# Kernel optimization log

Hardware: AMD Instinct MI355X
Metric: run time of the kernel (lower is better)

Reference implementation:

```python
import jax, jax.numpy as jnp
import numpy as np

B, S, D, H, L, V, DF = 2, 1024, 1024, 16, 4, 32000, 4096


def setup_inputs() -> dict:
    key = jax.random.key(0)
    ks = iter(jax.random.split(key, 64))
    rn = lambda shape, s=0.02: jax.random.normal(next(ks), shape, jnp.float32) * s
    inp = {
        'dec_input': rn((B, S, D), 1.0),
        'enc_input': rn((B, S, D), 1.0),
        # additive masks: causal for self-attn, none for cross-attn
        'masked_attention_mask': jnp.where(jnp.tril(jnp.ones((S, S), bool)), 0.0, -1e9)[None, None].astype(jnp.float32),
        'cross_attention_mask': jnp.zeros((1, 1, S, S), jnp.float32),
        'num_heads': H,
    }
    for p in ['sWq', 'sWk', 'sWv', 'sWo', 'cWq', 'cWk', 'cWv', 'cWo']:
        inp[p] = rn((L, D, D))
    for p in ['sbq', 'sbk', 'sbv', 'sbo', 'cbq', 'cbk', 'cbv', 'cbo']:
        inp[p] = jnp.zeros((L, D), jnp.float32)
    for p in ['ln1_g', 'ln2_g', 'ln3_g']:
        inp[p] = jnp.ones((L, D), jnp.float32)
    for p in ['ln1_b', 'ln2_b', 'ln3_b']:
        inp[p] = jnp.zeros((L, D), jnp.float32)
    inp['fW1'] = rn((L, D, DF)); inp['fb1'] = jnp.zeros((L, DF), jnp.float32)
    inp['fW2'] = rn((L, DF, D)); inp['fb2'] = jnp.zeros((L, D), jnp.float32)
    inp['Wout'] = rn((D, V)); inp['bout'] = jnp.zeros((V,), jnp.float32)
    return inp


def positional_encoding(seq_len, d_model, n=10000.0):
    # vectorized equivalent of the original triple-nested loop:
    # even d -> sin(i / n^(d/D)); odd d -> cos(i / n^((d-1)/D)); d==0 denom 1 == n^0
    i = jnp.arange(seq_len, dtype=jnp.float32)[:, None]
    d = jnp.arange(d_model)
    denom = jnp.power(n, (2 * (d // 2)).astype(jnp.float32) / d_model)
    ang = i / denom
    return jnp.where(d % 2 == 0, jnp.sin(ang), jnp.cos(ang))  # [S, D]


def layer_norm(x, g, b, eps=1e-5):
    m = jnp.mean(x, -1, keepdims=True)
    v = jnp.mean(jnp.square(x - m), -1, keepdims=True)
    return (x - m) * jax.lax.rsqrt(v + eps) * g + b


def mha(q_in, k_in, v_in, mask, Wq, bq, Wk, bk, Wv, bv, Wo, bo, h):
    b, sq, d = q_in.shape
    dh = d // h
    q = (q_in @ Wq + bq).reshape(b, sq, h, dh)
    k = (k_in @ Wk + bk).reshape(b, -1, h, dh)
    v = (v_in @ Wv + bv).reshape(b, -1, h, dh)
    scores = jnp.einsum('bqhd,bkhd->bhqk', q, k) / jnp.sqrt(jnp.float32(dh)) + mask
    attn = jax.nn.softmax(scores, axis=-1)
    out = jnp.einsum('bhqk,bkhd->bqhd', attn, v).reshape(b, sq, d)
    return out @ Wo + bo


def reference(dec_input, enc_input, masked_attention_mask, cross_attention_mask,
              sWq, sbq, sWk, sbk, sWv, sbv, sWo, sbo,
              cWq, cbq, cWk, cbk, cWv, cbv, cWo, cbo,
              ln1_g, ln1_b, ln2_g, ln2_b, ln3_g, ln3_b,
              fW1, fb1, fW2, fb2, Wout, bout, num_heads):
    b, s, d = dec_input.shape
    x0 = dec_input + positional_encoding(s, d)
    n_layers = sWq.shape[0]
    y = x0
    for l in range(n_layers):
        # NOTE: original DecoderSequential bug: every block consumes the ORIGINAL input;
        # only the last block's output survives.
        a1 = layer_norm(x0 + mha(x0, x0, x0, masked_attention_mask,
                                 sWq[l], sbq[l], sWk[l], sbk[l], sWv[l], sbv[l], sWo[l], sbo[l], num_heads),
                        ln1_g[l], ln1_b[l])
        a2 = layer_norm(a1 + mha(a1, enc_input, enc_input, cross_attention_mask,
                                 cWq[l], cbq[l], cWk[l], cbk[l], cWv[l], cbv[l], cWo[l], cbo[l], num_heads),
                        ln2_g[l], ln2_b[l])
        ff = jax.nn.relu(a2 @ fW1[l] + fb1[l]) @ fW2[l] + fb2[l]
        y = layer_norm(a2 + ff, ln3_g[l], ln3_b[l])
    return y @ Wout + bout  # [B, S, V]
```

## Files before the change

### kernel.cpp

```cpp
#include <hip/hip_runtime.h>
#include <cstdint>
#include <cstddef>

#define DEV __device__ __forceinline__

typedef __attribute__((ext_vector_type(8))) short short8;
typedef __attribute__((ext_vector_type(4))) float f32x4;
typedef __attribute__((ext_vector_type(16))) float f32x16;
typedef __attribute__((ext_vector_type(4))) unsigned short ushort4v;

DEV unsigned short f2bf(float f){
  union { float f; unsigned int i; } v; v.f = f;
  unsigned int r = v.i + 0x7fffu + ((v.i >> 16) & 1u);
  return (unsigned short)(r >> 16);
}

DEV void gld_lds16(const unsigned short* g, unsigned short* lds){
  __builtin_amdgcn_global_load_lds((const __attribute__((address_space(1))) void*)g,
                                   (__attribute__((address_space(3))) void*)lds, 16, 0, 0);
}

template<int BN, int EPI>
__global__ __launch_bounds__(256, 2)
void gemm32(const unsigned short* __restrict__ A,
            const unsigned short* __restrict__ Bt,
            const float* __restrict__ bias,
            void* __restrict__ C, int M, int N, int K)
{
  constexpr int NFR  = BN / 64;
  constexpr int ROWS = 128 + BN;
  constexpr int BUFH = ROWS * 32;
  constexpr int GLD  = ROWS / 64;
  __shared__ __align__(16) unsigned short lds[3 * BUFH];

  const int tid = threadIdx.x, wid = tid >> 6, l = tid & 63;
  const int wr = wid >> 1, wcn = wid & 1;

  const int nbm = M / 128, nbn = N / BN;
  const int nwg = nbm * nbn;
  const int q8 = nwg >> 3, r8 = nwg & 7;
  const int xcd = blockIdx.x & 7, within = blockIdx.x >> 3;
  const int wg = (xcd < r8 ? xcd * (q8 + 1) : r8 * (q8 + 1) + (xcd - r8) * q8) + within;
  const int mb = (wg % nbm) * 128, nb = (wg / nbm) * BN;

  const int nk = K / 32;

  const int r31 = l & 31, hi = l >> 5;
  const int so0 = (( hi)      ^ (r31 & 3)) * 8;
  const int so1 = ((2 + hi)   ^ (r31 & 3)) * 8;
  const int abase = (wr * 64 + r31) * 32;
  const int bbase = 4096 + (wcn * (BN / 2) + r31) * 32;

  f32x16 acc[2][NFR];
  #pragma unroll
  for (int m = 0; m < 2; m++)
    #pragma unroll
    for (int n = 0; n < NFR; n++)
      #pragma unroll
      for (int e = 0; e < 16; e++) acc[m][n][e] = 0.f;

#define STAGE_A(c, tt, bb) \
  gld_lds16(A + (size_t)(mb + (c)*64 + (tid>>2)) * K + (size_t)(tt)*32 + (((tid&3)^((tid>>2)&3))*8), \
            lds + (bb)*BUFH + (c)*2048 + tid*8)
#define STAGE_B(c, tt, bb) \
  gld_lds16(Bt + (size_t)(nb + (c)*64 + (tid>>2)) * K + (size_t)(tt)*32 + (((tid&3)^((tid>>2)&3))*8), \
            lds + (bb)*BUFH + 4096 + (c)*2048 + tid*8)
#define WAIT_GLD() do { if constexpr (GLD == 6) asm volatile("s_waitcnt vmcnt(6)" ::: "memory"); \
                        else                    asm volatile("s_waitcnt vmcnt(4)" ::: "memory"); } while(0)

  STAGE_A(0, 0, 0); STAGE_A(1, 0, 0);
  #pragma unroll
  for (int c = 0; c < NFR; c++) STAGE_B(c, 0, 0);
  if (nk > 1){
    STAGE_A(0, 1, 1); STAGE_A(1, 1, 1);
    #pragma unroll
    for (int c = 0; c < NFR; c++) STAGE_B(c, 1, 1);
    WAIT_GLD();
  } else {
    asm volatile("s_waitcnt vmcnt(0)" ::: "memory");
  }
  asm volatile("" ::: "memory");
  __builtin_amdgcn_s_barrier();
  asm volatile("" ::: "memory");

  int bb = 0;
  for (int u = 0; u < nk; u++){
    const unsigned short* buf = lds + bb * BUFH;
    const int sb = (bb >= 1) ? bb - 1 : 2;
    const bool st = (u + 2 < nk);
    short8 af[2], bf[NFR];

    af[0] = *(const short8*)(buf + abase + so0);
    af[1] = *(const short8*)(buf + abase + 1024 + so0);
    #pragma unroll
    for (int n = 0; n < NFR; n++) bf[n] = *(const short8*)(buf + bbase + n * 1024 + so0);
    if (st){
      STAGE_A(0, u + 2, sb); STAGE_A(1, u + 2, sb);
      if constexpr (NFR == 4) STAGE_B(0, u + 2, sb);
    }
    __builtin_amdgcn_s_setprio(1);
    #pragma unroll
    for (int m = 0; m < 2; m++)
      #pragma unroll
      for (int n = 0; n < NFR; n++)
        acc[m][n] = __builtin_amdgcn_mfma_f32_32x32x16_bf16(af[m], bf[n], acc[m][n], 0, 0, 0);
    __builtin_amdgcn_s_setprio(0);

    af[0] = *(const short8*)(buf + abase + so1);
    af[1] = *(const short8*)(buf + abase + 1024 + so1);
    #pragma unroll
    for (int n = 0; n < NFR; n++) bf[n] = *(const short8*)(buf + bbase + n * 1024 + so1);
    if (st){
      if constexpr (NFR == 4){ STAGE_B(1, u + 2, sb); STAGE_B(2, u + 2, sb); STAGE_B(3, u + 2, sb); }
      else                   { STAGE_B(0, u + 2, sb); STAGE_B(1, u + 2, sb); }
    }
    __builtin_amdgcn_s_setprio(1);
    #pragma unroll
    for (int m = 0; m < 2; m++)
      #pragma unroll
      for (int n = 0; n < NFR; n++)
        acc[m][n] = __builtin_amdgcn_mfma_f32_32x32x16_bf16(af[m], bf[n], acc[m][n], 0, 0, 0);
    __builtin_amdgcn_s_setprio(0);

    if (st)               WAIT_GLD();
    else if (u + 1 < nk)  asm volatile("s_waitcnt vmcnt(0)" ::: "memory");
    asm volatile("" ::: "memory");
    __builtin_amdgcn_s_barrier();
    asm volatile("" ::: "memory");
    bb = (bb == 2) ? 0 : bb + 1;
  }
#undef WAIT_GLD
#undef STAGE_A
#undef STAGE_B

  #pragma unroll
  for (int n = 0; n < NFR; n++){
    const int col = nb + wcn * (BN / 2) + n * 32 + r31;
    const float bv = bias ? bias[col] : 0.f;
    #pragma unroll
    for (int m = 0; m < 2; m++){
      const int rowb = mb + wr * 64 + m * 32 + 4 * hi;
      #pragma unroll
      for (int reg = 0; reg < 16; reg++){
        const int row = rowb + (reg & 3) + 8 * (reg >> 2);
        float v = acc[m][n][reg] + bv;
        size_t idx = (size_t)row * N + col;
        if (EPI == 0)       ((float*)C)[idx] = v;
        else if (EPI == 3)  __builtin_nontemporal_store(v, &((float*)C)[idx]);
        else if (EPI == 1)  ((unsigned short*)C)[idx] = f2bf(v);
        else { v = v > 0.f ? v : 0.f; ((unsigned short*)C)[idx] = f2bf(v); }
      }
    }
  }
}

template<int BM, int BN, int EPI>
__global__ __launch_bounds__(256, 2)
void gemm_bt(const unsigned short* __restrict__ A,
             const unsigned short* __restrict__ Bt,
             const float* __restrict__ bias,
             void* __restrict__ C, int M, int N, int K)
{
  constexpr int MF = BM / 32, NF = BN / 32;
  constexpr int LA = BM / 64, LB = BN / 64;
  __shared__ __align__(16) unsigned short lds[2 * (BM + BN) * 32];

  const int tid = threadIdx.x, w = tid >> 6, l = tid & 63;
  const int wr = w >> 1, wc = w & 1;

  const int nbm = M / BM, nbn = N / BN;
  const int nwg = nbm * nbn;
  const int q8 = nwg >> 3, r8 = nwg & 7;
  const int xcd = blockIdx.x & 7, within = blockIdx.x >> 3;
  const int wg = (xcd < r8 ? xcd * (q8 + 1) : r8 * (q8 + 1) + (xcd - r8) * q8) + within;
  const int mb = (wg % nbm) * BM, nb = (wg / nbm) * BN;

  unsigned short* As0 = lds;
  unsigned short* Bs0 = lds + BM * 32;
  unsigned short* As1 = lds + (BM + BN) * 32;
  unsigned short* Bs1 = As1 + BM * 32;

  f32x4 acc[MF][NF];
  #pragma unroll
  for (int m = 0; m < MF; m++)
    #pragma unroll
    for (int n = 0; n < NF; n++) acc[m][n] = (f32x4){0.f, 0.f, 0.f, 0.f};

  const int srow = l >> 2;
  const int scol = (((l & 3) ^ ((l >> 2) & 3) ^ ((l >> 4) & 3)) * 8);
  const int rswz = (l & 3) ^ ((l >> 2) & 3);

  #define STAGE(Ad, Bd, k0) do { \
    _Pragma("unroll") \
    for (int i = 0; i < LA; i++){ \
      int chunk = i * 4 + w; \
      gld_lds16(A + (size_t)(mb + chunk * 16 + srow) * K + (k0) + scol, (Ad) + chunk * 512); \
    } \
    _Pragma("unroll") \
    for (int i = 0; i < LB; i++){ \
      int chunk = i * 4 + w; \
      gld_lds16(Bt + (size_t)(nb + chunk * 16 + srow) * K + (k0) + scol, (Bd) + chunk * 512); \
    } } while(0)

  STAGE(As0, Bs0, 0);
  const int nk = K / 32;
  const int rdoff = ((l >> 4) ^ rswz) * 8;
  for (int kt = 0; kt < nk; kt++){
    __syncthreads();
    unsigned short* Ac = (kt & 1) ? As1 : As0;
    unsigned short* Bc = (kt & 1) ? Bs1 : Bs0;
    if (kt + 1 < nk){
      unsigned short* An = (kt & 1) ? As0 : As1;
      unsigned short* Bn = (kt & 1) ? Bs0 : Bs1;
      STAGE(An, Bn, (kt + 1) * 32);
    }
    short8 af[MF], bfr[NF];
    #pragma unroll
    for (int m = 0; m < MF; m++)
      af[m] = *(const short8*)(Ac + (wr * (BM / 2) + m * 16 + (l & 15)) * 32 + rdoff);
    #pragma unroll
    for (int n = 0; n < NF; n++)
      bfr[n] = *(const short8*)(Bc + (wc * (BN / 2) + n * 16 + (l & 15)) * 32 + rdoff);
    #pragma unroll
    for (int m = 0; m < MF; m++)
      #pragma unroll
      for (int n = 0; n < NF; n++)
        acc[m][n] = __builtin_amdgcn_mfma_f32_16x16x32_bf16(af[m], bfr[n], acc[m][n], 0, 0, 0);
  }
  #undef STAGE

  #pragma unroll
  for (int n = 0; n < NF; n++){
    const int col = nb + wc * (BN / 2) + n * 16 + (l & 15);
    const float bv = bias ? bias[col] : 0.f;
    #pragma unroll
    for (int m = 0; m < MF; m++){
      const int row0 = mb + wr * (BM / 2) + m * 16 + ((l >> 4) << 2);
      #pragma unroll
      for (int jj = 0; jj < 4; jj++){
        float v = acc[m][n][jj] + bv;
        size_t idx = (size_t)(row0 + jj) * N + col;
        if (EPI == 0)       ((float*)C)[idx] = v;
        else if (EPI == 3)  __builtin_nontemporal_store(v, &((float*)C)[idx]);
        else if (EPI == 1)  ((unsigned short*)C)[idx] = f2bf(v);
        else { v = v > 0.f ? v : 0.f; ((unsigned short*)C)[idx] = f2bf(v); }
      }
    }
  }
}

template<int CAUSAL>
__global__ __launch_bounds__(256)
void attn_kernel(const unsigned short* __restrict__ Qb, int ldq,
                 const unsigned short* __restrict__ Kb, int ldk,
                 const unsigned short* __restrict__ Vb, int ldv,
                 unsigned short* __restrict__ Ob, int ldo)
{
  constexpr int S = 1024;
  __shared__ __align__(16) unsigned short vt[64][40];
  __shared__ __align__(16) unsigned short plds[4][16][40];
  const int tid = threadIdx.x, w = tid >> 6, l = tid & 63;
  const int qt = blockIdx.x, bh = blockIdx.y;
  const int b = bh >> 4, h = bh & 15;
  const int hoff = h * 64;
  const size_t rb = (size_t)b * S;

  const int qrow = qt * 64 + w * 16 + (l & 15);
  const unsigned short* qp = Qb + (rb + qrow) * ldq + hoff + ((l >> 4) * 8);
  short8 qf0 = *(const short8*)qp;
  short8 qf1 = *(const short8*)(qp + 32);

  float m_run[4] = {-1e30f, -1e30f, -1e30f, -1e30f};
  float l_run[4] = {0.f, 0.f, 0.f, 0.f};
  f32x4 oacc[4];
  #pragma unroll
  for (int t = 0; t < 4; t++) oacc[t] = (f32x4){0.f, 0.f, 0.f, 0.f};

  const int qmax = qt * 64 + w * 16 + 15;
  const int nkeys = CAUSAL ? (qt * 64 + 64) : S;
  const int skey = tid >> 3, sd8 = (tid & 7) * 8;

  for (int kb = 0; kb < nkeys; kb += 32){
    short8 vv = *(const short8*)(Vb + (rb + kb + skey) * ldv + hoff + sd8);
    #pragma unroll
    for (int i = 0; i < 8; i++) vt[sd8 + i][skey] = (unsigned short)vv[i];
    __syncthreads();
    if (!CAUSAL || kb <= qmax){
      f32x4 sc[2];
      #pragma unroll
      for (int g = 0; g < 2; g++){
        const unsigned short* kp = Kb + (rb + kb + g * 16 + (l & 15)) * ldk + hoff + ((l >> 4) * 8);
        short8 kf0 = *(const short8*)kp;
        short8 kf1 = *(const short8*)(kp + 32);
        f32x4 z = (f32x4){0.f, 0.f, 0.f, 0.f};
        z = __builtin_amdgcn_mfma_f32_16x16x32_bf16(qf0, kf0, z, 0, 0, 0);
        z = __builtin_amdgcn_mfma_f32_16x16x32_bf16(qf1, kf1, z, 0, 0, 0);
        sc[g] = z;
      }
      #pragma unroll
      for (int jj = 0; jj < 4; jj++){
        float s0 = sc[0][jj] * 0.125f, s1 = sc[1][jj] * 0.125f;
        if (CAUSAL){
          int q = qt * 64 + w * 16 + ((l >> 4) << 2) + jj;
          if (kb + (l & 15) > q)      s0 = -1e30f;
          if (kb + 16 + (l & 15) > q) s1 = -1e30f;
        }
        float mx = fmaxf(s0, s1);
        mx = fmaxf(mx, __shfl_xor(mx, 1));
        mx = fmaxf(mx, __shfl_xor(mx, 2));
        mx = fmaxf(mx, __shfl_xor(mx, 4));
        mx = fmaxf(mx, __shfl_xor(mx, 8));
        float mnew = fmaxf(m_run[jj], mx);
        float scal = __expf(m_run[jj] - mnew);
        m_run[jj] = mnew;
        float p0 = __expf(s0 - mnew), p1 = __expf(s1 - mnew);
        float rs = p0 + p1;
        rs += __shfl_xor(rs, 1); rs += __shfl_xor(rs, 2);
        rs += __shfl_xor(rs, 4); rs += __shfl_xor(rs, 8);
        l_run[jj] = l_run[jj] * scal + rs;
        #pragma unroll
        for (int t = 0; t < 4; t++) oacc[t][jj] *= scal;
        int qr = ((l >> 4) << 2) + jj;
        plds[w][qr][l & 15]      = f2bf(p0);
        plds[w][qr][16 + (l & 15)] = f2bf(p1);
      }
      asm volatile("s_waitcnt lgkmcnt(0)" ::: "memory");
      short8 pf = *(const short8*)&plds[w][l & 15][(l >> 4) * 8];
      #pragma unroll
      for (int t = 0; t < 4; t++){
        short8 vf = *(const short8*)&vt[t * 16 + (l & 15)][(l >> 4) * 8];
        oacc[t] = __builtin_amdgcn_mfma_f32_16x16x32_bf16(pf, vf, oacc[t], 0, 0, 0);
      }
    }
    __syncthreads();
  }
  #pragma unroll
  for (int jj = 0; jj < 4; jj++){
    float inv = 1.f / l_run[jj];
    int q = qt * 64 + w * 16 + ((l >> 4) << 2) + jj;
    #pragma unroll
    for (int t = 0; t < 4; t++)
      Ob[(rb + q) * ldo + hoff + t * 16 + (l & 15)] = f2bf(oacc[t][jj] * inv);
  }
}

__global__ __launch_bounds__(256)
void ln_kernel(const float* __restrict__ x1, const float* __restrict__ x2,
               const float* __restrict__ g, const float* __restrict__ be,
               float* __restrict__ outf, unsigned short* __restrict__ outb)
{
  const int row = blockIdx.x, t = threadIdx.x;
  __shared__ float red[4];
  const float4 v1 = ((const float4*)(x1 + (size_t)row * 1024))[t];
  const float4 v2 = ((const float4*)(x2 + (size_t)row * 1024))[t];
  float x[4] = {v1.x + v2.x, v1.y + v2.y, v1.z + v2.z, v1.w + v2.w};
  float s = x[0] + x[1] + x[2] + x[3];
  for (int o = 1; o < 64; o <<= 1) s += __shfl_xor(s, o);
  const int w = t >> 6, l = t & 63;
  if (l == 0) red[w] = s;
  __syncthreads();
  const float mean = (red[0] + red[1] + red[2] + red[3]) * (1.f / 1024.f);
  float d[4]; float sq = 0.f;
  #pragma unroll
  for (int i = 0; i < 4; i++){ d[i] = x[i] - mean; sq += d[i] * d[i]; }
  __syncthreads();
  for (int o = 1; o < 64; o <<= 1) sq += __shfl_xor(sq, o);
  if (l == 0) red[w] = sq;
  __syncthreads();
  const float var = (red[0] + red[1] + red[2] + red[3]) * (1.f / 1024.f);
  const float inv = rsqrtf(var + 1e-5f);
  const int base = t * 4;
  #pragma unroll
  for (int i = 0; i < 4; i++){
    float o = d[i] * inv * g[base + i] + be[base + i];
    if (outf) outf[(size_t)row * 1024 + base + i] = o;
    outb[(size_t)row * 1024 + base + i] = f2bf(o);
  }
}

__global__ __launch_bounds__(256)
void build_x0(const float* __restrict__ dec, float* __restrict__ xf, unsigned short* __restrict__ xb)
{
  const int i = blockIdx.x * 256 + threadIdx.x;
  const int i4 = i * 4;
  const int d0 = i4 & 1023;
  const int s  = (i4 >> 10) & 1023;
  float4 dv = ((const float4*)dec)[i];
  const float* dvp = (const float*)&dv;
  float o[4];
  #pragma unroll
  for (int j = 0; j < 4; j++){
    int dd = d0 + j;
    float e = (float)(dd & ~1) * (1.f / 1024.f);
    float den = expf(e * 9.210340371976184f);
    float ang = (float)s / den;
    float pe = (dd & 1) ? cosf(ang) : sinf(ang);
    o[j] = dvp[j] + pe;
  }
  ((float4*)xf)[i] = make_float4(o[0], o[1], o[2], o[3]);
  ushort4v ob; ob[0] = f2bf(o[0]); ob[1] = f2bf(o[1]); ob[2] = f2bf(o[2]); ob[3] = f2bf(o[3]);
  ((ushort4v*)xb)[i] = ob;
}

__global__ __launch_bounds__(256)
void cvt_bf16_k(const float* __restrict__ in, unsigned short* __restrict__ out)
{
  const int i = blockIdx.x * 256 + threadIdx.x;
  float4 v = ((const float4*)in)[i];
  ushort4v o; o[0] = f2bf(v.x); o[1] = f2bf(v.y); o[2] = f2bf(v.z); o[3] = f2bf(v.w);
  ((ushort4v*)out)[i] = o;
}

__global__ __launch_bounds__(256)
void transpose_cvt(const float* __restrict__ in, unsigned short* __restrict__ out, int R, int C)
{
  __shared__ float t[32][33];
  const int cb = blockIdx.x * 32, rbk = blockIdx.y * 32;
  const int tx = threadIdx.x & 31, ty = threadIdx.x >> 5;
  #pragma unroll
  for (int i = 0; i < 4; i++)
    t[ty + 8 * i][tx] = in[(size_t)(rbk + ty + 8 * i) * C + cb + tx];
  __syncthreads();
  #pragma unroll
  for (int i = 0; i < 4; i++){
    int c = ty + 8 * i;
    out[(size_t)(cb + c) * R + rbk + tx] = f2bf(t[tx][c]);
  }
}

struct TPtrs { const float* src[8]; unsigned short* dst[8]; };
__global__ __launch_bounds__(256)
void transpose_cvt8(TPtrs p)
{
  __shared__ float t[32][33];
  const float* __restrict__ in = p.src[blockIdx.z];
  unsigned short* __restrict__ out = p.dst[blockIdx.z];
  const int cb = blockIdx.x * 32, rbk = blockIdx.y * 32;
  const int tx = threadIdx.x & 31, ty = threadIdx.x >> 5;
  #pragma unroll
  for (int i = 0; i < 4; i++)
    t[ty + 8 * i][tx] = in[(size_t)(rbk + ty + 8 * i) * 1024 + cb + tx];
  __syncthreads();
  #pragma unroll
  for (int i = 0; i < 4; i++){
    int c = ty + 8 * i;
    out[(size_t)(cb + c) * 1024 + rbk + tx] = f2bf(t[tx][c]);
  }
}

__global__ __launch_bounds__(256)
void copy_biases(const float* sbq, const float* sbk, const float* sbv,
                 const float* cbk, const float* cbv,
                 float* bqkv, float* bkvc)
{
  const int i = blockIdx.x * 256 + threadIdx.x;
  const int seg = i >> 10, off = i & 1023;
  if (seg == 0)      bqkv[off] = sbq[off];
  else if (seg == 1) bqkv[1024 + off] = sbk[off];
  else if (seg == 2) bqkv[2048 + off] = sbv[off];
  else if (seg == 3) bkvc[off] = cbk[off];
  else               bkvc[1024 + off] = cbv[off];
}

extern "C" void kernel_launch(void* const* d_in, const int* in_sizes, int n_in,
                              void* d_out, int out_size, void* d_ws, size_t ws_size,
                              hipStream_t stream)
{
  constexpr int S = 1024, D = 1024, V = 32000, DF = 4096;
  constexpr int M = 2 * S;
  constexpr int DD = D * D;
  constexpr int l3 = 3;

  const float* dec  = (const float*)d_in[0];
  const float* enc  = (const float*)d_in[1];
  const float* sWq = (const float*)d_in[5]  + l3 * DD;
  const float* sWk = (const float*)d_in[6]  + l3 * DD;
  const float* sWv = (const float*)d_in[7]  + l3 * DD;
  const float* sWo = (const float*)d_in[8]  + l3 * DD;
  const float* cWq = (const float*)d_in[9]  + l3 * DD;
  const float* cWk = (const float*)d_in[10] + l3 * DD;
  const float* cWv = (const float*)d_in[11] + l3 * DD;
  const float* cWo = (const float*)d_in[12] + l3 * DD;
  const float* sbq = (const float*)d_in[13] + l3 * D;
  const float* sbk = (const float*)d_in[14] + l3 * D;
  const float* sbv = (const float*)d_in[15] + l3 * D;
  const float* sbo = (const float*)d_in[16] + l3 * D;
  const float* cbq = (const float*)d_in[17] + l3 * D;
  const float* cbk = (const float*)d_in[18] + l3 * D;
  const float* cbv = (const float*)d_in[19] + l3 * D;
  const float* cbo = (const float*)d_in[20] + l3 * D;
  const float* ln1g = (const float*)d_in[21] + l3 * D;
  const float* ln2g = (const float*)d_in[22] + l3 * D;
  const float* ln3g = (const float*)d_in[23] + l3 * D;
  const float* ln1b = (const float*)d_in[24] + l3 * D;
  const float* ln2b = (const float*)d_in[25] + l3 * D;
  const float* ln3b = (const float*)d_in[26] + l3 * D;
  const float* fW1 = (const float*)d_in[27] + (size_t)l3 * D * DF;
  const float* fb1 = (const float*)d_in[28] + l3 * DF;
  const float* fW2 = (const float*)d_in[29] + (size_t)l3 * DF * D;
  const float* fb2 = (const float*)d_in[30] + l3 * D;
  const float* Wout = (const float*)d_in[31];
  const float* bout = (const float*)d_in[32];
  float* out = (float*)d_out;

  uint8_t* wsp = (uint8_t*)d_ws;
  auto alloc = [&](size_t bytes) -> void* {
    void* p = wsp; wsp += (bytes + 255) & ~(size_t)255; return p;
  };
  float*          x0f  = (float*)alloc((size_t)M * D * 4);
  unsigned short* x0b  = (unsigned short*)alloc((size_t)M * D * 2);
  unsigned short* encb = (unsigned short*)alloc((size_t)M * D * 2);
  unsigned short* wqkv = (unsigned short*)alloc((size_t)3 * DD * 2);
  unsigned short* wos  = (unsigned short*)alloc((size_t)DD * 2);
  unsigned short* wqc  = (unsigned short*)alloc((size_t)DD * 2);
  unsigned short* wkvc = (unsigned short*)alloc((size_t)2 * DD * 2);
  unsigned short* woc  = (unsigned short*)alloc((size_t)DD * 2);
  unsigned short* wf1  = (unsigned short*)alloc((size_t)D * DF * 2);
  unsigned short* wf2  = (unsigned short*)alloc((size_t)D * DF * 2);
  unsigned short* wvo  = (unsigned short*)alloc((size_t)V * D * 2);
  float*          bqkv = (float*)alloc(3 * D * 4);
  float*          bkvc = (float*)alloc(2 * D * 4);
  unsigned short* qkv  = (unsigned short*)alloc((size_t)M * 3 * D * 2);
  unsigned short* attnb= (unsigned short*)alloc((size_t)M * D * 2);
  float*          oproj= (float*)alloc((size_t)M * D * 4);
  float*          a1f  = (float*)alloc((size_t)M * D * 4);
  unsigned short* a1b  = (unsigned short*)alloc((size_t)M * D * 2);
  unsigned short* qc   = (unsigned short*)alloc((size_t)M * D * 2);
  unsigned short* kvc  = (unsigned short*)alloc((size_t)M * 2 * D * 2);
  float*          a2f  = (float*)alloc((size_t)M * D * 4);
  unsigned short* a2b  = (unsigned short*)alloc((size_t)M * D * 2);
  unsigned short* ffh  = (unsigned short*)alloc((size_t)M * DF * 2);
  unsigned short* yb   = (unsigned short*)alloc((size_t)M * D * 2);

  build_x0<<<M * D / 4 / 256, 256, 0, stream>>>(dec, x0f, x0b);
  cvt_bf16_k<<<M * D / 4 / 256, 256, 0, stream>>>(enc, encb);

  TPtrs tp;
  tp.src[0] = sWq; tp.dst[0] = wqkv;
  tp.src[1] = sWk; tp.dst[1] = wqkv + DD;
  tp.src[2] = sWv; tp.dst[2] = wqkv + 2 * DD;
  tp.src[3] = sWo; tp.dst[3] = wos;
  tp.src[4] = cWq; tp.dst[4] = wqc;
  tp.src[5] = cWk; tp.dst[5] = wkvc;
  tp.src[6] = cWv; tp.dst[6] = wkvc + DD;
  tp.src[7] = cWo; tp.dst[7] = woc;
  transpose_cvt8<<<dim3(32, 32, 8), 256, 0, stream>>>(tp);
  transpose_cvt<<<dim3(DF/32, D/32), 256, 0, stream>>>(fW1, wf1, D, DF);
  transpose_cvt<<<dim3(D/32, DF/32), 256, 0, stream>>>(fW2, wf2, DF, D);
  transpose_cvt<<<dim3(V/32, D/32), 256, 0, stream>>>(Wout, wvo, D, V);
  copy_biases<<<20, 256, 0, stream>>>(sbq, sbk, sbv, cbk, cbv, bqkv, bkvc);

  gemm32<128,1><<<(M/128)*(3*D/128), 256, 0, stream>>>(x0b, wqkv, bqkv, qkv, M, 3*D, D);
  attn_kernel<1><<<dim3(S/64, 32), 256, 0, stream>>>(qkv, 3*D, qkv + D, 3*D, qkv + 2*D, 3*D, attnb, D);
  gemm_bt<64,64,0><<<(M/64)*(D/64), 256, 0, stream>>>(attnb, wos, sbo, oproj, M, D, D);
  ln_kernel<<<M, 256, 0, stream>>>(x0f, oproj, ln1g, ln1b, a1f, a1b);

  gemm_bt<64,64,1><<<(M/64)*(D/64), 256, 0, stream>>>(a1b, wqc, cbq, qc, M, D, D);
  gemm32<128,1><<<(M/128)*(2*D/128), 256, 0, stream>>>(encb, wkvc, bkvc, kvc, M, 2*D, D);
  attn_kernel<0><<<dim3(S/64, 32), 256, 0, stream>>>(qc, D, kvc, 2*D, kvc + D, 2*D, attnb, D);
  gemm_bt<64,64,0><<<(M/64)*(D/64), 256, 0, stream>>>(attnb, woc, cbo, oproj, M, D, D);
  ln_kernel<<<M, 256, 0, stream>>>(a1f, oproj, ln2g, ln2b, a2f, a2b);

  gemm32<128,2><<<(M/128)*(DF/128), 256, 0, stream>>>(a2b, wf1, fb1, ffh, M, DF, D);
  gemm_bt<64,128,0><<<(M/64)*(D/128), 256, 0, stream>>>(ffh, wf2, fb2, oproj, M, D, DF);
  ln_kernel<<<M, 256, 0, stream>>>(a2f, oproj, ln3g, ln3b, nullptr, yb);

  gemm32<256,3><<<(M/128)*(V/256), 256, 0, stream>>>(yb, wvo, bout, out, M, V, D);
}
```

Measured before the change: 623.7 us.

## Unify GEMMs on gemm32 with new LDS swizzle, drop gemm_bt, widen transposes

```diff
diff --git a/kernel.cpp b/kernel.cpp
--- a/kernel.cpp
+++ b/kernel.cpp
@@ -18,6 +18,12 @@
 DEV void gld_lds16(const unsigned short* g, unsigned short* lds){
   __builtin_amdgcn_global_load_lds((const __attribute__((address_space(1))) void*)g,
                                    (__attribute__((address_space(3))) void*)lds, 16, 0, 0);
+}
+
+DEV int swz(int r, int s){
+  int ln = r >> 1;
+  int sl = ((r & 1) << 2) | s;
+  return ln * 64 + (((sl ^ (ln & 7))) << 3);
 }
 
 template<int BN, int EPI>
@@ -45,11 +51,26 @@
 
   const int nk = K / 32;
 
+  const int sL   = tid >> 3;
+  const int sSl  = (tid & 7) ^ (sL & 7);
+  const int sRow = sL * 2 + (sSl >> 2);
+  const int sKc  = (sSl & 3) * 8;
+
   const int r31 = l & 31, hi = l >> 5;
-  const int so0 = (( hi)      ^ (r31 & 3)) * 8;
-  const int so1 = ((2 + hi)   ^ (r31 & 3)) * 8;
-  const int abase = (wr * 64 + r31) * 32;
-  const int bbase = 4096 + (wcn * (BN / 2) + r31) * 32;
+
+  int aoff[2][2], boff[NFR][2];
+  #pragma unroll
+  for (int m = 0; m < 2; m++)
+    #pragma unroll
+    for (int ks = 0; ks < 2; ks++)
+      aoff[m][ks] = wr * 2048 + swz(m * 32 + r31, 2 * ks + hi);
+  #pragma unroll
+  for (int n = 0; n < NFR; n++){
+    const int col = wcn * (BN / 2) + n * 32 + r31;
+    #pragma unroll
+    for (int ks = 0; ks < 2; ks++)
+      boff[n][ks] = 4096 + (col >> 6) * 2048 + swz(col & 63, 2 * ks + hi);
+  }
 
   f32x16 acc[2][NFR];
   #pragma unroll
@@ -59,14 +80,15 @@
       #pragma unroll
       for (int e = 0; e < 16; e++) acc[m][n][e] = 0.f;
 
-#define STAGE_A(c, tt, bb) \
-  gld_lds16(A + (size_t)(mb + (c)*64 + (tid>>2)) * K + (size_t)(tt)*32 + (((tid&3)^((tid>>2)&3))*8), \
-            lds + (bb)*BUFH + (c)*2048 + tid*8)
-#define STAGE_B(c, tt, bb) \
-  gld_lds16(Bt + (size_t)(nb + (c)*64 + (tid>>2)) * K + (size_t)(tt)*32 + (((tid&3)^((tid>>2)&3))*8), \
-            lds + (bb)*BUFH + 4096 + (c)*2048 + tid*8)
+#define STAGE_A(c, tt, b2) \
+  gld_lds16(A + (size_t)(mb + (c)*64 + sRow) * K + (size_t)(tt)*32 + sKc, \
+            lds + (b2)*BUFH + (c)*2048 + tid*8)
+#define STAGE_B(c, tt, b2) \
+  gld_lds16(Bt + (size_t)(nb + (c)*64 + sRow) * K + (size_t)(tt)*32 + sKc, \
+            lds + (b2)*BUFH + 4096 + (c)*2048 + tid*8)
 #define WAIT_GLD() do { if constexpr (GLD == 6) asm volatile("s_waitcnt vmcnt(6)" ::: "memory"); \
-                        else                    asm volatile("s_waitcnt vmcnt(4)" ::: "memory"); } while(0)
+                        else if constexpr (GLD == 4) asm volatile("s_waitcnt vmcnt(4)" ::: "memory"); \
+                        else asm volatile("s_waitcnt vmcnt(3)" ::: "memory"); } while(0)
 
   STAGE_A(0, 0, 0); STAGE_A(1, 0, 0);
   #pragma unroll
@@ -90,10 +112,10 @@
     const bool st = (u + 2 < nk);
     short8 af[2], bf[NFR];
 
-    af[0] = *(const short8*)(buf + abase + so0);
-    af[1] = *(const short8*)(buf + abase + 1024 + so0);
-    #pragma unroll
-    for (int n = 0; n < NFR; n++) bf[n] = *(const short8*)(buf + bbase + n * 1024 + so0);
+    af[0] = *(const short8*)(buf + aoff[0][0]);
+    af[1] = *(const short8*)(buf + aoff[1][0]);
+    #pragma unroll
+    for (int n = 0; n < NFR; n++) bf[n] = *(const short8*)(buf + boff[n][0]);
     if (st){
       STAGE_A(0, u + 2, sb); STAGE_A(1, u + 2, sb);
       if constexpr (NFR == 4) STAGE_B(0, u + 2, sb);
@@ -106,13 +128,14 @@
         acc[m][n] = __builtin_amdgcn_mfma_f32_32x32x16_bf16(af[m], bf[n], acc[m][n], 0, 0, 0);
     __builtin_amdgcn_s_setprio(0);
 
-    af[0] = *(const short8*)(buf + abase + so1);
-    af[1] = *(const short8*)(buf + abase + 1024 + so1);
-    #pragma unroll
-    for (int n = 0; n < NFR; n++) bf[n] = *(const short8*)(buf + bbase + n * 1024 + so1);
+    af[0] = *(const short8*)(buf + aoff[0][1]);
+    af[1] = *(const short8*)(buf + aoff[1][1]);
+    #pragma unroll
+    for (int n = 0; n < NFR; n++) bf[n] = *(const short8*)(buf + boff[n][1]);
     if (st){
       if constexpr (NFR == 4){ STAGE_B(1, u + 2, sb); STAGE_B(2, u + 2, sb); STAGE_B(3, u + 2, sb); }
-      else                   { STAGE_B(0, u + 2, sb); STAGE_B(1, u + 2, sb); }
+      else if constexpr (NFR == 2){ STAGE_B(0, u + 2, sb); STAGE_B(1, u + 2, sb); }
+      else { STAGE_B(0, u + 2, sb); }
     }
     __builtin_amdgcn_s_setprio(1);
     #pragma unroll
@@ -145,101 +168,6 @@
         const int row = rowb + (reg & 3) + 8 * (reg >> 2);
         float v = acc[m][n][reg] + bv;
         size_t idx = (size_t)row * N + col;
-        if (EPI == 0)       ((float*)C)[idx] = v;
-        else if (EPI == 3)  __builtin_nontemporal_store(v, &((float*)C)[idx]);
-        else if (EPI == 1)  ((unsigned short*)C)[idx] = f2bf(v);
-        else { v = v > 0.f ? v : 0.f; ((unsigned short*)C)[idx] = f2bf(v); }
-      }
-    }
-  }
-}
-
-template<int BM, int BN, int EPI>
-__global__ __launch_bounds__(256, 2)
-void gemm_bt(const unsigned short* __restrict__ A,
-             const unsigned short* __restrict__ Bt,
-             const float* __restrict__ bias,
-             void* __restrict__ C, int M, int N, int K)
-{
-  constexpr int MF = BM / 32, NF = BN / 32;
-  constexpr int LA = BM / 64, LB = BN / 64;
-  __shared__ __align__(16) unsigned short lds[2 * (BM + BN) * 32];
-
-  const int tid = threadIdx.x, w = tid >> 6, l = tid & 63;
-  const int wr = w >> 1, wc = w & 1;
-
-  const int nbm = M / BM, nbn = N / BN;
-  const int nwg = nbm * nbn;
-  const int q8 = nwg >> 3, r8 = nwg & 7;
-  const int xcd = blockIdx.x & 7, within = blockIdx.x >> 3;
-  const int wg = (xcd < r8 ? xcd * (q8 + 1) : r8 * (q8 + 1) + (xcd - r8) * q8) + within;
-  const int mb = (wg % nbm) * BM, nb = (wg / nbm) * BN;
-
-  unsigned short* As0 = lds;
-  unsigned short* Bs0 = lds + BM * 32;
-  unsigned short* As1 = lds + (BM + BN) * 32;
-  unsigned short* Bs1 = As1 + BM * 32;
-
-  f32x4 acc[MF][NF];
-  #pragma unroll
-  for (int m = 0; m < MF; m++)
-    #pragma unroll
-    for (int n = 0; n < NF; n++) acc[m][n] = (f32x4){0.f, 0.f, 0.f, 0.f};
-
-  const int srow = l >> 2;
-  const int scol = (((l & 3) ^ ((l >> 2) & 3) ^ ((l >> 4) & 3)) * 8);
-  const int rswz = (l & 3) ^ ((l >> 2) & 3);
-
-  #define STAGE(Ad, Bd, k0) do { \
-    _Pragma("unroll") \
-    for (int i = 0; i < LA; i++){ \
-      int chunk = i * 4 + w; \
-      gld_lds16(A + (size_t)(mb + chunk * 16 + srow) * K + (k0) + scol, (Ad) + chunk * 512); \
-    } \
-    _Pragma("unroll") \
-    for (int i = 0; i < LB; i++){ \
-      int chunk = i * 4 + w; \
-      gld_lds16(Bt + (size_t)(nb + chunk * 16 + srow) * K + (k0) + scol, (Bd) + chunk * 512); \
-    } } while(0)
-
-  STAGE(As0, Bs0, 0);
-  const int nk = K / 32;
-  const int rdoff = ((l >> 4) ^ rswz) * 8;
-  for (int kt = 0; kt < nk; kt++){
-    __syncthreads();
-    unsigned short* Ac = (kt & 1) ? As1 : As0;
-    unsigned short* Bc = (kt & 1) ? Bs1 : Bs0;
-    if (kt + 1 < nk){
-      unsigned short* An = (kt & 1) ? As0 : As1;
-      unsigned short* Bn = (kt & 1) ? Bs0 : Bs1;
-      STAGE(An, Bn, (kt + 1) * 32);
-    }
-    short8 af[MF], bfr[NF];
-    #pragma unroll
-    for (int m = 0; m < MF; m++)
-      af[m] = *(const short8*)(Ac + (wr * (BM / 2) + m * 16 + (l & 15)) * 32 + rdoff);
-    #pragma unroll
-    for (int n = 0; n < NF; n++)
-      bfr[n] = *(const short8*)(Bc + (wc * (BN / 2) + n * 16 + (l & 15)) * 32 + rdoff);
-    #pragma unroll
-    for (int m = 0; m < MF; m++)
-      #pragma unroll
-      for (int n = 0; n < NF; n++)
-        acc[m][n] = __builtin_amdgcn_mfma_f32_16x16x32_bf16(af[m], bfr[n], acc[m][n], 0, 0, 0);
-  }
-  #undef STAGE
-
-  #pragma unroll
-  for (int n = 0; n < NF; n++){
-    const int col = nb + wc * (BN / 2) + n * 16 + (l & 15);
-    const float bv = bias ? bias[col] : 0.f;
-    #pragma unroll
-    for (int m = 0; m < MF; m++){
-      const int row0 = mb + wr * (BM / 2) + m * 16 + ((l >> 4) << 2);
-      #pragma unroll
-      for (int jj = 0; jj < 4; jj++){
-        float v = acc[m][n][jj] + bv;
-        size_t idx = (size_t)(row0 + jj) * N + col;
         if (EPI == 0)       ((float*)C)[idx] = v;
         else if (EPI == 3)  __builtin_nontemporal_store(v, &((float*)C)[idx]);
         else if (EPI == 1)  ((unsigned short*)C)[idx] = f2bf(v);
@@ -414,17 +342,18 @@
 __global__ __launch_bounds__(256)
 void transpose_cvt(const float* __restrict__ in, unsigned short* __restrict__ out, int R, int C)
 {
-  __shared__ float t[32][33];
-  const int cb = blockIdx.x * 32, rbk = blockIdx.y * 32;
+  __shared__ float t[32][65];
+  const int cb = blockIdx.x * 32, rb = blockIdx.y * 64;
   const int tx = threadIdx.x & 31, ty = threadIdx.x >> 5;
   #pragma unroll
-  for (int i = 0; i < 4; i++)
-    t[ty + 8 * i][tx] = in[(size_t)(rbk + ty + 8 * i) * C + cb + tx];
+  for (int i = 0; i < 8; i++)
+    t[tx][ty + 8 * i] = in[(size_t)(rb + ty + 8 * i) * C + cb + tx];
   __syncthreads();
-  #pragma unroll
-  for (int i = 0; i < 4; i++){
-    int c = ty + 8 * i;
-    out[(size_t)(cb + c) * R + rbk + tx] = f2bf(t[tx][c]);
+  const int lane = threadIdx.x & 63, cr = threadIdx.x >> 6;
+  #pragma unroll
+  for (int j = 0; j < 8; j++){
+    int c = cr + 4 * j;
+    out[(size_t)(cb + c) * R + rb + lane] = f2bf(t[c][lane]);
   }
 }
 
@@ -432,19 +361,20 @@
 __global__ __launch_bounds__(256)
 void transpose_cvt8(TPtrs p)
 {
-  __shared__ float t[32][33];
+  __shared__ float t[32][65];
   const float* __restrict__ in = p.src[blockIdx.z];
   unsigned short* __restrict__ out = p.dst[blockIdx.z];
-  const int cb = blockIdx.x * 32, rbk = blockIdx.y * 32;
+  const int cb = blockIdx.x * 32, rb = blockIdx.y * 64;
   const int tx = threadIdx.x & 31, ty = threadIdx.x >> 5;
   #pragma unroll
-  for (int i = 0; i < 4; i++)
-    t[ty + 8 * i][tx] = in[(size_t)(rbk + ty + 8 * i) * 1024 + cb + tx];
+  for (int i = 0; i < 8; i++)
+    t[tx][ty + 8 * i] = in[(size_t)(rb + ty + 8 * i) * 1024 + cb + tx];
   __syncthreads();
-  #pragma unroll
-  for (int i = 0; i < 4; i++){
-    int c = ty + 8 * i;
-    out[(size_t)(cb + c) * 1024 + rbk + tx] = f2bf(t[tx][c]);
+  const int lane = threadIdx.x & 63, cr = threadIdx.x >> 6;
+  #pragma unroll
+  for (int j = 0; j < 8; j++){
+    int c = cr + 4 * j;
+    out[(size_t)(cb + c) * 1024 + rb + lane] = f2bf(t[c][lane]);
   }
 }
 
@@ -544,25 +474,25 @@
   tp.src[5] = cWk; tp.dst[5] = wkvc;
   tp.src[6] = cWv; tp.dst[6] = wkvc + DD;
   tp.src[7] = cWo; tp.dst[7] = woc;
-  transpose_cvt8<<<dim3(32, 32, 8), 256, 0, stream>>>(tp);
-  transpose_cvt<<<dim3(DF/32, D/32), 256, 0, stream>>>(fW1, wf1, D, DF);
-  transpose_cvt<<<dim3(D/32, DF/32), 256, 0, stream>>>(fW2, wf2, DF, D);
-  transpose_cvt<<<dim3(V/32, D/32), 256, 0, stream>>>(Wout, wvo, D, V);
+  transpose_cvt8<<<dim3(32, 16, 8), 256, 0, stream>>>(tp);
+  transpose_cvt<<<dim3(DF/32, D/64), 256, 0, stream>>>(fW1, wf1, D, DF);
+  transpose_cvt<<<dim3(D/32, DF/64), 256, 0, stream>>>(fW2, wf2, DF, D);
+  transpose_cvt<<<dim3(V/32, D/64), 256, 0, stream>>>(Wout, wvo, D, V);
   copy_biases<<<20, 256, 0, stream>>>(sbq, sbk, sbv, cbk, cbv, bqkv, bkvc);
 
   gemm32<128,1><<<(M/128)*(3*D/128), 256, 0, stream>>>(x0b, wqkv, bqkv, qkv, M, 3*D, D);
   attn_kernel<1><<<dim3(S/64, 32), 256, 0, stream>>>(qkv, 3*D, qkv + D, 3*D, qkv + 2*D, 3*D, attnb, D);
-  gemm_bt<64,64,0><<<(M/64)*(D/64), 256, 0, stream>>>(attnb, wos, sbo, oproj, M, D, D);
+  gemm32<64,0><<<(M/128)*(D/64), 256, 0, stream>>>(attnb, wos, sbo, oproj, M, D, D);
   ln_kernel<<<M, 256, 0, stream>>>(x0f, oproj, ln1g, ln1b, a1f, a1b);
 
-  gemm_bt<64,64,1><<<(M/64)*(D/64), 256, 0, stream>>>(a1b, wqc, cbq, qc, M, D, D);
+  gemm32<64,1><<<(M/128)*(D/64), 256, 0, stream>>>(a1b, wqc, cbq, qc, M, D, D);
   gemm32<128,1><<<(M/128)*(2*D/128), 256, 0, stream>>>(encb, wkvc, bkvc, kvc, M, 2*D, D);
   attn_kernel<0><<<dim3(S/64, 32), 256, 0, stream>>>(qc, D, kvc, 2*D, kvc + D, 2*D, attnb, D);
-  gemm_bt<64,64,0><<<(M/64)*(D/64), 256, 0, stream>>>(attnb, woc, cbo, oproj, M, D, D);
+  gemm32<64,0><<<(M/128)*(D/64), 256, 0, stream>>>(attnb, woc, cbo, oproj, M, D, D);
   ln_kernel<<<M, 256, 0, stream>>>(a1f, oproj, ln2g, ln2b, a2f, a2b);
 
-  gemm32<128,2><<<(M/128)*(DF/128), 256, 0, stream>>>(a2b, wf1, fb1, ffh, M, DF, D);
-  gemm_bt<64,128,0><<<(M/64)*(D/128), 256, 0, stream>>>(ffh, wf2, fb2, oproj, M, D, DF);
+  gemm32<256,2><<<(M/128)*(DF/256), 256, 0, stream>>>(a2b, wf1, fb1, ffh, M, DF, D);
+  gemm32<64,0><<<(M/128)*(D/64), 256, 0, stream>>>(ffh, wf2, fb2, oproj, M, D, DF);
   ln_kernel<<<M, 256, 0, stream>>>(a2f, oproj, ln3g, ln3b, nullptr, yb);
 
   gemm32<256,3><<<(M/128)*(V/256), 256, 0, stream>>>(yb, wvo, bout, out, M, V, D);
```

Result: faster. 603.6 us (-3.2%).
